# Kernel tuning notes

Hardware: AMD Instinct MI355X
Metric: run time of the kernel (lower is better)

## Reference

```python
import jax, jax.numpy as jnp
import numpy as np

B, T, D, H = 2, 1024, 1024, 16
K = D            # key_dim = hidden * expand_k (1.0)
V = 2 * D        # value_dim = hidden * expand_v (2.0)
DK, DV = K // H, V // H
I = 2816         # SwiGLU intermediate
CONV = 4
EPS = 1e-6


def rmsnorm(x, w, eps=EPS):
    return x * jax.lax.rsqrt(jnp.mean(x * x, -1, keepdims=True) + eps) * w


def l2norm(x, eps=EPS):
    return x * jax.lax.rsqrt(jnp.sum(x * x, -1, keepdims=True) + eps)


def short_conv(x, w):
    # depthwise causal conv1d (kernel CONV, no bias) + silu; x [B,T,C], w [C,CONV]
    kern = w.T[:, None, :]  # [CONV, 1, C]
    y = jax.lax.conv_general_dilated(
        x, kern, (1,), [(CONV - 1, 0)],
        dimension_numbers=('NWC', 'WIO', 'NWC'),
        feature_group_count=x.shape[-1])
    return jax.nn.silu(y)


def setup_inputs() -> dict:
    key = jax.random.key(0)
    ks = jax.random.split(key, 20)
    p = lambda i, shape, s=0.02: jax.random.normal(ks[i], shape, jnp.float32) * s
    return dict(
        x=jax.random.normal(ks[0], (B, T, D), jnp.float32),
        norm1_w=jnp.ones((D,), jnp.float32),
        wq=p(1, (D, K)), wk=p(2, (D, K)), wv=p(3, (D, V)),
        conv_q=p(4, (K, CONV), 0.3), conv_k=p(5, (K, CONV), 0.3), conv_v=p(6, (V, CONV), 0.3),
        wb=p(7, (D, H)), wa=p(8, (D, H)),
        A_log=jnp.log(jax.random.uniform(ks[9], (H,), jnp.float32, 1.0, 16.0)),
        dt_bias=jnp.log(jnp.expm1(jax.random.uniform(ks[10], (H,), jnp.float32, 0.001, 0.1))),
        wg=p(11, (D, V)),
        o_norm_w=jnp.ones((DV,), jnp.float32),
        wo=p(12, (V, D)),
        norm2_w=jnp.ones((D,), jnp.float32),
        w1=p(13, (D, I)), w2=p(14, (I, D)), w3=p(15, (D, I)),
    )


def reference(x, norm1_w, wq, wk, wv, conv_q, conv_k, conv_v, wb, wa,
              A_log, dt_bias, wg, o_norm_w, wo, norm2_w, w1, w2, w3):
    h = rmsnorm(x, norm1_w)
    # projections + short causal conv (silu)
    q = short_conv(h @ wq, conv_q).reshape(B, T, H, DK)
    k = short_conv(h @ wk, conv_k).reshape(B, T, H, DK)
    v = short_conv(h @ wv, conv_v).reshape(B, T, H, DV)
    q = l2norm(q) * (DK ** -0.5)
    k = l2norm(k)
    beta = jax.nn.sigmoid(h @ wb)                              # [B,T,H]
    # mamba-style decay gate: g = -exp(A_log) * softplus(a + dt_bias)
    g = -jnp.exp(A_log) * jax.nn.softplus(h @ wa + dt_bias)   # [B,T,H]

    # gated delta rule: S_t = exp(g_t)*S_{t-1}; u_t = beta_t*(v_t - k_t^T S_t);
    # S_t += k_t u_t^T; o_t = q_t^T S_t
    def step(S, inp):
        qt, kt, vt, gt, bt = inp                               # [B,H,*]
        S = S * jnp.exp(gt)[..., None, None]
        u = (vt - jnp.einsum('bhk,bhkv->bhv', kt, S)) * bt[..., None]
        S = S + kt[..., None] * u[:, :, None, :]
        ot = jnp.einsum('bhk,bhkv->bhv', qt, S)
        return S, ot

    S0 = jnp.zeros((B, H, DK, DV), x.dtype)
    seq = (q.transpose(1, 0, 2, 3), k.transpose(1, 0, 2, 3),
           v.transpose(1, 0, 2, 3), g.transpose(1, 0, 2), beta.transpose(1, 0, 2))
    _, o = jax.lax.scan(step, S0, seq)
    o = o.transpose(1, 0, 2, 3)                                # [B,T,H,DV]

    # output gate: per-head RMSNorm * swish(gate), then out-projection
    gate = (h @ wg).reshape(B, T, H, DV)
    o = rmsnorm(o, o_norm_w) * gate * jax.nn.sigmoid(gate)
    x = x + o.reshape(B, T, V) @ wo

    # SwiGLU MLP with residual
    h2 = rmsnorm(x, norm2_w)
    return x + (jax.nn.silu(h2 @ w1) * (h2 @ w3)) @ w2
```

## Files before the change

### kernel.cpp

```cpp
#include <hip/hip_runtime.h>
#include <stdint.h>

typedef unsigned short u16;
typedef float f32x4 __attribute__((ext_vector_type(4)));
typedef __bf16 bf16x8 __attribute__((ext_vector_type(8)));
typedef unsigned short u16x8 __attribute__((ext_vector_type(8)));

#define N1P 6400

__device__ __forceinline__ u16 f2bf(float f) {
    union { float f; uint32_t u; } v; v.f = f;
    uint32_t u = v.u;
    return (u16)((u + 0x7FFFu + ((u >> 16) & 1u)) >> 16);
}
__device__ __forceinline__ float bf2f(u16 h) {
    union { uint32_t u; float f; } v; v.u = ((uint32_t)h) << 16; return v.f;
}
__device__ __forceinline__ float sigm(float x) { return 1.f / (1.f + __expf(-x)); }

__device__ __forceinline__ void async16(const u16* g, u16* l) {
    __builtin_amdgcn_global_load_lds((const __attribute__((address_space(1))) void*)g,
                                     (__attribute__((address_space(3))) void*)l, 16, 0, 0);
}

__device__ __forceinline__ int swz64(int row, int col) {
    return row * 128 + ((((col >> 3) ^ (row & 7)) << 3) + (col & 7)) * 2;
}
__device__ __forceinline__ bf16x8 frag64(const u16* m, int rowbase, int lane, int kk) {
    const int row = rowbase + (lane & 15);
    const int unit = (lane >> 4) + (kk << 2);
    return *(const bf16x8*)((const char*)m + row * 128 + ((unit ^ (row & 7)) << 4));
}

struct TJob { const float* src; u16* dst; int rows, cols, rowOff, rowStride, nOut, blkBase, gx, mode; };
struct TJobs { TJob j[10]; };

__global__ __launch_bounds__(256) void k_transpose_all(TJobs jobs, int njobs) {
    __shared__ float tile[64][33];
    const int bid = blockIdx.x;
    int ji = 0;
#pragma unroll
    for (int i = 1; i < 10; ++i)
        if (i < njobs && bid >= jobs.j[i].blkBase) ji = i;
    const TJob J = jobs.j[ji];
    const int bx = bid - J.blkBase;
    const int n0 = (bx % J.gx) * 32, k0 = (bx / J.gx) * 64;
    const int tid = threadIdx.x;
    const int tx = tid & 31, ty = tid >> 5;
    const int c = n0 + tx;
    const bool cok = (c < J.cols);
#pragma unroll
    for (int i = 0; i < 8; ++i) {
        const int r = k0 + i * 8 + ty;
        tile[i * 8 + ty][tx] = cok ? J.src[(size_t)r * J.cols + c] : 0.f;
    }
    __syncthreads();
    const int n = tid >> 3, seg = tid & 7;
    const int ng = n0 + n;
    if (ng < J.nOut) {
        u16x8 o;
#pragma unroll
        for (int e = 0; e < 8; ++e) o[e] = f2bf(tile[seg * 8 + e][n]);
        const int drow = (J.mode == 0) ? (J.rowOff + ng * J.rowStride)
                                       : (J.rowOff + ((ng >> 4) << 5) + (ng & 15));
        *(u16x8*)&J.dst[(size_t)drow * J.rows + k0 + seg * 8] = o;
    }
}

__global__ __launch_bounds__(256) void k_rmsnorm(const float* __restrict__ x, const float* __restrict__ w,
                                                 u16* __restrict__ out) {
    const int row = blockIdx.x, tid = threadIdx.x, lane = tid & 63, wave = tid >> 6;
    const float4 v = ((const float4*)(x + (size_t)row * 1024))[tid];
    float ss = v.x * v.x + v.y * v.y + v.z * v.z + v.w * v.w;
#pragma unroll
    for (int o = 1; o < 64; o <<= 1) ss += __shfl_xor(ss, o);
    __shared__ float sred[4];
    if (lane == 0) sred[wave] = ss;
    __syncthreads();
    const float tot = sred[0] + sred[1] + sred[2] + sred[3];
    const float rn = rsqrtf(tot * (1.f / 1024.f) + 1e-6f);
    const float4 wv = ((const float4*)w)[tid];
    uint2 pk;
    pk.x = (uint32_t)f2bf(v.x * rn * wv.x) | ((uint32_t)f2bf(v.y * rn * wv.y) << 16);
    pk.y = (uint32_t)f2bf(v.z * rn * wv.z) | ((uint32_t)f2bf(v.w * rn * wv.w) << 16);
    *(uint2*)&out[(size_t)row * 1024 + tid * 4] = pk;
}

template <int EPI>
__global__ __launch_bounds__(512, 2) void k_gemm256(const u16* __restrict__ A, const u16* __restrict__ Bt,
                                                    u16* __restrict__ Cout, int N, int Kd) {
    __shared__ __align__(16) u16 L[65536];
    const int q8 = (int)gridDim.x >> 3;
    const int bid = blockIdx.x;
    const int wg = (bid & 7) * q8 + (bid >> 3);
    const int bm = wg & 7, bn = wg >> 3;
    const int tid = threadIdx.x, lane = tid & 63, wave = tid >> 6;
    const int wm = wave >> 2, wn = wave & 3;

    const int scol = ((tid & 7) ^ ((tid >> 3) & 7)) * 8;
    const u16* gA = A + (size_t)(bm * 256 + (tid >> 3)) * Kd + scol;
    const u16* gB = Bt + (size_t)(bn * 256 + (tid >> 3)) * Kd + scol;
    u16* dstT = L + tid * 8;

    const int NT = Kd >> 6;
    const int NI = NT >> 1;

    auto issue = [&](const u16* g, int mtx, int kt, int h) {
        u16* d = dstT + (kt & 1) * 32768 + mtx * 16384 + h * 8192;
        const u16* s = g + (size_t)(h * 128) * Kd + kt * 64;
        async16(s, d);
        async16(s + (size_t)64 * Kd, d + 4096);
    };

    issue(gB, 1, 0, 0); issue(gB, 1, 0, 1);
    issue(gA, 0, 0, 0); issue(gA, 0, 0, 1);
    issue(gB, 1, 1, 0); issue(gB, 1, 1, 1);
    asm volatile("s_waitcnt vmcnt(4)" ::: "memory");
    __builtin_amdgcn_s_barrier();

    f32x4 acc[8][4] = {};
    bf16x8 bq[4][2];

    for (int i = 0; i < NI; ++i) {
        const int kt0 = 2 * i;
#pragma unroll
        for (int p = 0; p < 8; ++p) {
            const int half = p >> 2;
            const int q = p & 3;
            const u16* Ab = L + half * 32768;
            const u16* Bb = L + half * 32768 + 16384;
            if (q == 0) {
#pragma unroll
                for (int ni = 0; ni < 4; ++ni)
#pragma unroll
                    for (int kk = 0; kk < 2; ++kk)
                        bq[ni][kk] = frag64(Bb, wn * 64 + ni * 16, lane, kk);
            }
            bf16x8 af[2][2];
#pragma unroll
            for (int j = 0; j < 2; ++j)
#pragma unroll
                for (int kk = 0; kk < 2; ++kk)
                    af[j][kk] = frag64(Ab, wm * 128 + (2 * q + j) * 16, lane, kk);
            if (p == 0) { if (kt0 + 1 < NT) issue(gA, 0, kt0 + 1, 0); }
            if (p == 1) { if (kt0 + 1 < NT) issue(gA, 0, kt0 + 1, 1);
                          if (kt0 + 2 < NT) issue(gB, 1, kt0 + 2, 0); }
            if (p == 2) { if (kt0 + 2 < NT) issue(gB, 1, kt0 + 2, 1); }
            if (p == 4) { if (kt0 + 2 < NT) issue(gA, 0, kt0 + 2, 0); }
            if (p == 5) { if (kt0 + 2 < NT) issue(gA, 0, kt0 + 2, 1);
                          if (kt0 + 3 < NT) issue(gB, 1, kt0 + 3, 0); }
            if (p == 6) { if (kt0 + 3 < NT) issue(gB, 1, kt0 + 3, 1); }
            if (p == 3) { if (i + 1 < NI) { asm volatile("s_waitcnt vmcnt(4)" ::: "memory"); }
                          else            { asm volatile("s_waitcnt vmcnt(0)" ::: "memory"); } }
            if (p == 7) { if (i + 1 < NI) { asm volatile("s_waitcnt vmcnt(4)" ::: "memory"); } }
            __builtin_amdgcn_s_barrier();
            __builtin_amdgcn_s_setprio(1);
#pragma unroll
            for (int j = 0; j < 2; ++j)
#pragma unroll
                for (int ni = 0; ni < 4; ++ni)
#pragma unroll
                    for (int kk = 0; kk < 2; ++kk)
                        acc[2 * q + j][ni] = __builtin_amdgcn_mfma_f32_16x16x32_bf16(
                            af[j][kk], bq[ni][kk], acc[2 * q + j][ni], 0, 0, 0);
            __builtin_amdgcn_s_setprio(0);
            __builtin_amdgcn_s_barrier();
        }
    }

    const int rsub = (lane >> 4) * 4, csub = lane & 15;
    if constexpr (EPI == 2) {
        u16* ct = L;
#pragma unroll
        for (int r = 0; r < 2; ++r) {
            if (wm == r) {
#pragma unroll
                for (int mi = 0; mi < 8; ++mi)
#pragma unroll
                    for (int ni = 0; ni < 4; ++ni)
#pragma unroll
                        for (int rr = 0; rr < 4; ++rr)
                            ct[(mi * 16 + rsub + rr) * 264 + wn * 64 + ni * 16 + csub] =
                                f2bf(acc[mi][ni][rr]);
            }
            __syncthreads();
#pragma unroll
            for (int k = 0; k < 8; ++k) {
                const int f = (tid + k * 512) * 8;
                const int r2 = f >> 8, c = f & 255;
                *(u16x8*)&Cout[(size_t)(bm * 256 + r * 128 + r2) * N + bn * 256 + c] =
                    *(const u16x8*)&ct[r2 * 264 + c];
            }
            __syncthreads();
        }
    } else {
        u16* ct = L;
#pragma unroll
        for (int mi = 0; mi < 8; ++mi)
#pragma unroll
            for (int g = 0; g < 2; ++g)
#pragma unroll
                for (int rr = 0; rr < 4; ++rr) {
                    const float u1 = acc[mi][2 * g][rr];
                    const float u3 = acc[mi][2 * g + 1][rr];
                    ct[(wm * 128 + mi * 16 + rsub + rr) * 132 + wn * 32 + g * 16 + csub] =
                        f2bf(u1 * sigm(u1) * u3);
                }
        __syncthreads();
#pragma unroll
        for (int k = 0; k < 8; ++k) {
            const int f = (tid + k * 512) * 8;
            const int r2 = f >> 7, c = f & 127;
            *(u16x8*)&Cout[(size_t)(bm * 256 + r2) * N + bn * 128 + c] =
                *(const u16x8*)&ct[r2 * 132 + c];
        }
    }
}

__global__ __launch_bounds__(512) void k_gemm_skinny(const u16* __restrict__ A, const u16* __restrict__ Bt,
                                                     float* __restrict__ Cout, const float* __restrict__ Res,
                                                     int N, int Kd) {
    __shared__ __align__(16) char smem[49152];
    u16* Asb = (u16*)smem;
    u16* Bsb = (u16*)(smem + 32768);
    const int q = (int)gridDim.x >> 3;
    const int bid = blockIdx.x;
    const int wg = (bid & 7) * q + (bid >> 3);
    const int bm = wg & 15, bn = wg >> 4;
    const int tid = threadIdx.x, lane = tid & 63, wave = tid >> 6;
    const int wm = wave >> 1, wn = wave & 1;

    const int srow = tid >> 3;
    const int scol = ((tid & 7) ^ ((tid >> 3) & 7)) * 8;
    const u16* gA = A + (size_t)(bm * 128 + srow) * Kd + scol;
    const u16* gB = Bt + (size_t)(bn * 64 + srow) * Kd + scol;

    f32x4 acc[2][2] = {};
    const int NT = Kd >> 6;

    async16(gA, Asb + wave * 512);
    async16(gA + (size_t)64 * Kd, Asb + 4096 + wave * 512);
    async16(gB, Bsb + wave * 512);
    asm volatile("s_waitcnt vmcnt(0)" ::: "memory");
    __syncthreads();

    int buf = 0;
    for (int t = 0; t < NT; ++t) {
        if (t + 1 < NT) {
            const int k0 = (t + 1) << 6;
            const int ba = (buf ^ 1) * 8192, bb2 = (buf ^ 1) * 4096;
            async16(gA + k0, Asb + ba + wave * 512);
            async16(gA + (size_t)64 * Kd + k0, Asb + ba + 4096 + wave * 512);
            async16(gB + k0, Bsb + bb2 + wave * 512);
        }
        const u16* Ab = Asb + buf * 8192;
        const u16* Bb = Bsb + buf * 4096;
#pragma unroll
        for (int kk = 0; kk < 2; ++kk) {
            bf16x8 af[2], bfr[2];
#pragma unroll
            for (int mi = 0; mi < 2; ++mi) af[mi] = frag64(Ab, wm * 32 + mi * 16, lane, kk);
#pragma unroll
            for (int ni = 0; ni < 2; ++ni) bfr[ni] = frag64(Bb, wn * 32 + ni * 16, lane, kk);
#pragma unroll
            for (int mi = 0; mi < 2; ++mi)
#pragma unroll
                for (int ni = 0; ni < 2; ++ni)
                    acc[mi][ni] = __builtin_amdgcn_mfma_f32_16x16x32_bf16(af[mi], bfr[ni], acc[mi][ni], 0, 0, 0);
        }
        asm volatile("s_waitcnt vmcnt(0)" ::: "memory");
        __syncthreads();
        buf ^= 1;
    }

    const int rsub = (lane >> 4) * 4;
    const int csub = lane & 15;
    float* ctile = (float*)smem;
#pragma unroll
    for (int mi = 0; mi < 2; ++mi)
#pragma unroll
        for (int ni = 0; ni < 2; ++ni)
#pragma unroll
            for (int r = 0; r < 4; ++r)
                ctile[(wm * 32 + mi * 16 + rsub + r) * 68 + wn * 32 + ni * 16 + csub] = acc[mi][ni][r];
    __syncthreads();
#pragma unroll
    for (int k = 0; k < 4; ++k) {
        const int f = (tid + k * 512) * 4;
        const int r = f >> 6, c = f & 63;
        float4 v = *(const float4*)&ctile[r * 68 + c];
        const float4 rv = *(const float4*)&Res[(size_t)(bm * 128 + r) * N + bn * 64 + c];
        v.x += rv.x; v.y += rv.y; v.z += rv.z; v.w += rv.w;
        *(float4*)&Cout[(size_t)(bm * 128 + r) * N + bn * 64 + c] = v;
    }
}

__global__ __launch_bounds__(256) void k_scan1(
    const u16* __restrict__ P, const float* __restrict__ cwq, const float* __restrict__ cwk,
    const float* __restrict__ cwv, const float* __restrict__ A_log, const float* __restrict__ dtb,
    u16* __restrict__ CHW, u16* __restrict__ CHM, u16* __restrict__ CHQc,
    u16* __restrict__ CHKcT, u16* __restrict__ CHU0T, float* __restrict__ CHcC,
    u16* __restrict__ CHA2m, u16* __restrict__ CHB) {
    __shared__ __align__(16) char sm[66048];
    u16* Ql   = (u16*)(sm);
    u16* Kl   = (u16*)(sm + 8192);
    u16* VTb  = (u16*)(sm + 16384);
    u16* KT1b = (u16*)(sm + 32768);
    u16* Mim  = (u16*)(sm + 40960);
    u16* MTim = (u16*)(sm + 49152);
    u16* Tb   = (u16*)(sm + 57344);
    float* Tl    = (float*)sm;
    float* gcs   = (float*)(sm + 65536);
    float* betal = (float*)(sm + 65792);
    u16* Vtmp = Mim;

    const int blk = blockIdx.x;
    const int bb = blk >> 8, h = (blk >> 4) & 15, ch = blk & 15;
    const int bhc = blk;
    const int tid = threadIdx.x, lane = tid & 63, wave = tid >> 6;
    const long rowbase = (long)bb * 1024 + ch * 64;

    if (tid < 64) {
        const long pr = (rowbase + tid) * (long)N1P;
        betal[tid] = sigm(bf2f(P[pr + 4096 + h]));
        const float a = bf2f(P[pr + 4112 + h]) + dtb[h];
        const float sp = (a > 15.f) ? a : log1pf(__expf(a));
        gcs[tid] = -__expf(A_log[h]) * sp;
    }
    {
        const int g = tid & 31, rb2 = tid >> 5;
        int colbase; const float* cw;
        if (g < 8)       { const int cc = h * 64 + g * 8;        colbase = cc;        cw = cwq + cc * 4; }
        else if (g < 16) { const int cc = h * 64 + (g - 8) * 8;   colbase = 1024 + cc; cw = cwk + cc * 4; }
        else             { const int cc = h * 128 + (g - 16) * 8; colbase = 2048 + cc; cw = cwv + cc * 4; }
        float4 wgt[8];
#pragma unroll
        for (int e = 0; e < 8; ++e) wgt[e] = ((const float4*)cw)[e];
        u16x8 taps[11];
#pragma unroll
        for (int j = 0; j < 11; ++j) {
            const int tloc = ch * 64 + rb2 * 8 - 3 + j;
            if (tloc >= 0) taps[j] = *(const u16x8*)&P[((long)bb * 1024 + tloc) * N1P + colbase];
            else           taps[j] = u16x8{};
        }
#pragma unroll
        for (int r = 0; r < 8; ++r) {
            float y[8];
            float ss = 0.f;
#pragma unroll
            for (int e = 0; e < 8; ++e) {
                float v = bf2f(taps[r][e]) * wgt[e].x + bf2f(taps[r + 1][e]) * wgt[e].y +
                          bf2f(taps[r + 2][e]) * wgt[e].z + bf2f(taps[r + 3][e]) * wgt[e].w;
                v = v * sigm(v);
                y[e] = v;
                ss += v * v;
            }
            ss += __shfl_xor(ss, 1); ss += __shfl_xor(ss, 2); ss += __shfl_xor(ss, 4);
            const float rn = rsqrtf(ss + 1e-6f);
            const float sc = (g < 8) ? rn * 0.125f : (g < 16 ? rn : 1.f);
            u16x8 o;
#pragma unroll
            for (int e = 0; e < 8; ++e) o[e] = f2bf(y[e] * sc);
            const int row = rb2 * 8 + r;
            if (g < 16) {
                u16* dst = (g < 8) ? Ql : Kl;
                *(u16x8*)((char*)dst + row * 128 + (((g & 7) ^ (row & 7)) << 4)) = o;
            } else {
                *(u16x8*)&Vtmp[row * 128 + (g - 16) * 8] = o;
            }
        }
    }
    __syncthreads();

    if (wave == 0) {
        float g = gcs[lane];
#pragma unroll
        for (int off = 1; off < 64; off <<= 1) {
            float n = __shfl_up(g, off, 64);
            if (lane >= off) g += n;
        }
        gcs[lane] = g;
    }
    for (int u = tid; u < 1024; u += 256) {
        int r = u >> 4, c8 = u & 15;
        u16x8 vv = *(const u16x8*)&Vtmp[r * 128 + c8 * 8];
        float bsc = betal[r];
#pragma unroll
        for (int j = 0; j < 8; ++j) {
            int dv = c8 * 8 + j;
            *(u16*)((char*)VTb + swz64(dv, r)) = f2bf(bf2f(vv[j]) * bsc);
        }
    }
    f32x4 aQK[4] = {}, aKK[4] = {};
#pragma unroll
    for (int nt = 0; nt < 4; ++nt)
#pragma unroll
        for (int kk = 0; kk < 2; ++kk) {
            bf16x8 bq = frag64(Kl, nt * 16, lane, kk);
            aQK[nt] = __builtin_amdgcn_mfma_f32_16x16x32_bf16(frag64(Ql, wave * 16, lane, kk), bq, aQK[nt], 0, 0, 0);
            aKK[nt] = __builtin_amdgcn_mfma_f32_16x16x32_bf16(frag64(Kl, wave * 16, lane, kk), bq, aKK[nt], 0, 0, 0);
        }
    __syncthreads();

    const float gcsC = gcs[63];
    float am[4][4];
#pragma unroll
    for (int nt = 0; nt < 4; ++nt)
#pragma unroll
        for (int reg = 0; reg < 4; ++reg) {
            int t = wave * 16 + ((lane >> 4) << 2) + reg;
            int i = nt * 16 + (lane & 15);
            float dec = __expf(gcs[t] - gcs[i]);
            float mv = (i <= t) ? dec * aQK[nt][reg] : 0.f;
            *(u16*)((char*)CHM + (size_t)bhc * 8192 + swz64(t, i)) = f2bf(mv);
            float a = (i < t) ? betal[t] * dec * aKK[nt][reg] : 0.f;
            am[nt][reg] = -a;
            u16 amb = f2bf(-a);
            *(u16*)((char*)Mim + swz64(t, i)) = amb;
            *(u16*)((char*)MTim + swz64(i, t)) = amb;
        }
    for (int e = tid; e < 4096; e += 256) {
        int r = e >> 6, c = e & 63;
        int ib = swz64(r, c);
        float qv = bf2f(*(const u16*)((const char*)Ql + ib)) * __expf(gcs[r]);
        *(u16*)((char*)CHQc + (size_t)bhc * 8192 + ib) = f2bf(qv);
        float kv = bf2f(*(const u16*)((const char*)Kl + ib));
        int ob = swz64(c, r);
        *(u16*)((char*)KT1b + ob) = f2bf(kv * betal[r] * __expf(gcs[r]));
        *(u16*)((char*)CHKcT + (size_t)bhc * 8192 + ob) = f2bf(kv * __expf(gcsC - gcs[r]));
    }
    if (tid == 0) CHcC[bhc] = __expf(gcsC);
    __syncthreads();

#pragma unroll
    for (int nt = 0; nt < 4; ++nt)
#pragma unroll
        for (int reg = 0; reg < 4; ++reg) {
            int t = wave * 16 + ((lane >> 4) << 2) + reg;
            int i = nt * 16 + (lane & 15);
            float tv = (t == i) ? 1.f : am[nt][reg];
            Tl[t * 64 + i] = tv;
            *(u16*)((char*)Tb + swz64(t, i)) = f2bf(tv);
        }
    __syncthreads();

    const int hi = wave * 16 + 15;
#pragma unroll
    for (int j = 1; j <= 5; ++j) {
        f32x4 aM[4] = {};
#pragma unroll
        for (int nt = 0; nt < 4; ++nt) {
            if (nt * 16 > hi - (1 << j)) continue;
#pragma unroll
            for (int kk = 0; kk < 2; ++kk) {
                if (kk * 32 > hi) break;
                aM[nt] = __builtin_amdgcn_mfma_f32_16x16x32_bf16(
                    frag64(Mim, wave * 16, lane, kk), frag64(MTim, nt * 16, lane, kk), aM[nt], 0, 0, 0);
            }
        }
        __syncthreads();
#pragma unroll
        for (int nt = 0; nt < 4; ++nt)
#pragma unroll
            for (int reg = 0; reg < 4; ++reg) {
                int t = wave * 16 + ((lane >> 4) << 2) + reg;
                int i = nt * 16 + (lane & 15);
                float mv = (t - i >= (1 << j)) ? aM[nt][reg] : 0.f;
                u16 mb = f2bf(mv);
                *(u16*)((char*)Mim + swz64(t, i)) = mb;
                *(u16*)((char*)MTim + swz64(i, t)) = mb;
            }
        __syncthreads();
        f32x4 aT[4];
#pragma unroll
        for (int nt = 0; nt < 4; ++nt)
#pragma unroll
            for (int reg = 0; reg < 4; ++reg) {
                int t = wave * 16 + ((lane >> 4) << 2) + reg;
                int i = nt * 16 + (lane & 15);
                aT[nt][reg] = Tl[t * 64 + i];
            }
#pragma unroll
        for (int nt = 0; nt < 4; ++nt) {
            if (nt * 16 > hi - (1 << j)) continue;
#pragma unroll
            for (int kk = 0; kk < 2; ++kk) {
                if (kk * 32 > hi) break;
                aT[nt] = __builtin_amdgcn_mfma_f32_16x16x32_bf16(
                    frag64(Tb, wave * 16, lane, kk), frag64(MTim, nt * 16, lane, kk), aT[nt], 0, 0, 0);
            }
        }
#pragma unroll
        for (int nt = 0; nt < 4; ++nt)
#pragma unroll
            for (int reg = 0; reg < 4; ++reg) {
                int t = wave * 16 + ((lane >> 4) << 2) + reg;
                int i = nt * 16 + (lane & 15);
                Tl[t * 64 + i] = aT[nt][reg];
                *(u16*)((char*)Tb + swz64(t, i)) = f2bf(aT[nt][reg]);
            }
    }
    __syncthreads();

    u16* KcTl = Ql;
    u16* WTl  = Kl;
    u16* U0Tl = Mim;
#pragma unroll
    for (int r = 0; r < 2; ++r) {
        const int g = r * 256 + tid;
        async16(CHKcT + (size_t)bhc * 4096 + (size_t)g * 8, KcTl + g * 8);
    }

    {
        f32x4 aW[4] = {};
#pragma unroll
        for (int nt = 0; nt < 4; ++nt)
#pragma unroll
            for (int kk = 0; kk < 2; ++kk) {
                if (kk * 32 > hi) break;
                aW[nt] = __builtin_amdgcn_mfma_f32_16x16x32_bf16(
                    frag64(Tb, wave * 16, lane, kk), frag64(KT1b, nt * 16, lane, kk), aW[nt], 0, 0, 0);
            }
#pragma unroll
        for (int nt = 0; nt < 4; ++nt)
#pragma unroll
            for (int reg = 0; reg < 4; ++reg) {
                int r = wave * 16 + ((lane >> 4) << 2) + reg;
                int c = nt * 16 + (lane & 15);
                u16 wv = f2bf(aW[nt][reg]);
                *(u16*)((char*)CHW + (size_t)bhc * 8192 + swz64(r, c)) = wv;
                *(u16*)((char*)WTl + swz64(c, r)) = wv;
            }
    }
#pragma unroll
    for (int rt = 0; rt < 2; ++rt) {
        f32x4 aU[4] = {};
        int rb = (wave * 2 + rt) * 16;
#pragma unroll
        for (int nt = 0; nt < 4; ++nt)
#pragma unroll
            for (int kk = 0; kk < 2; ++kk) {
                if (kk * 32 > nt * 16 + 15) continue;
                aU[nt] = __builtin_amdgcn_mfma_f32_16x16x32_bf16(
                    frag64(VTb, rb, lane, kk), frag64(Tb, nt * 16, lane, kk), aU[nt], 0, 0, 0);
            }
#pragma unroll
        for (int nt = 0; nt < 4; ++nt)
#pragma unroll
            for (int reg = 0; reg < 4; ++reg) {
                int dv = rb + ((lane >> 4) << 2) + reg;
                int c = nt * 16 + (lane & 15);
                u16 uv = f2bf(aU[nt][reg]);
                *(u16*)((char*)CHU0T + (size_t)bhc * 16384 + swz64(dv, c)) = uv;
                *(u16*)((char*)U0Tl + swz64(dv, c)) = uv;
            }
    }
    asm volatile("s_waitcnt vmcnt(0)" ::: "memory");
    __syncthreads();

    {
        f32x4 aA[4] = {};
#pragma unroll
        for (int nt = 0; nt < 4; ++nt)
#pragma unroll
            for (int kk = 0; kk < 2; ++kk)
                aA[nt] = __builtin_amdgcn_mfma_f32_16x16x32_bf16(
                    frag64(WTl, wave * 16, lane, kk), frag64(KcTl, nt * 16, lane, kk), aA[nt], 0, 0, 0);
#pragma unroll
        for (int nt = 0; nt < 4; ++nt)
#pragma unroll
            for (int reg = 0; reg < 4; ++reg) {
                int kI = wave * 16 + ((lane >> 4) << 2) + reg;
                int dk = nt * 16 + (lane & 15);
                *(u16*)((char*)CHA2m + (size_t)bhc * 8192 + swz64(dk, kI)) = f2bf(-aA[nt][reg]);
            }
    }
#pragma unroll
    for (int rt = 0; rt < 2; ++rt) {
        f32x4 aB[4] = {};
        int rb = (wave * 2 + rt) * 16;
#pragma unroll
        for (int nt = 0; nt < 4; ++nt)
#pragma unroll
            for (int kk = 0; kk < 2; ++kk)
                aB[nt] = __builtin_amdgcn_mfma_f32_16x16x32_bf16(
                    frag64(U0Tl, rb, lane, kk), frag64(KcTl, nt * 16, lane, kk), aB[nt], 0, 0, 0);
#pragma unroll
        for (int nt = 0; nt < 4; ++nt)
#pragma unroll
            for (int reg = 0; reg < 4; ++reg) {
                int dv = rb + ((lane >> 4) << 2) + reg;
                int dk = nt * 16 + (lane & 15);
                *(u16*)((char*)CHB + (size_t)bhc * 16384 + swz64(dv, dk)) = f2bf(aB[nt][reg]);
            }
    }
}

__global__ __launch_bounds__(256) void k_scan2(
    const u16* __restrict__ CHA2m, const u16* __restrict__ CHB,
    const float* __restrict__ CHcC, u16* __restrict__ CHS0) {
    __shared__ __align__(16) u16 stg[2][8192];
    __shared__ __align__(16) u16 STb[4096];
    __shared__ float ST[64 * 66];
    const int blk = blockIdx.x;
    const int bb = blk >> 5, h = (blk >> 1) & 15, dvh = blk & 1;
    const int bh = bb * 16 + h;
    const int tid = threadIdx.x, lane = tid & 63, wave = tid >> 6;

    for (int e = tid; e < 64 * 66; e += 256) ST[e] = 0.f;
    for (int e = tid; e < 4096; e += 256) STb[e] = 0;

    auto stage = [&](int buf, int ch) {
        const size_t base = (size_t)(bh * 16 + ch);
        const u16* sA = CHA2m + base * 4096;
        const u16* sB = CHB + base * 8192 + dvh * 4096;
#pragma unroll
        for (int r = 0; r < 2; ++r) {
            const int g = r * 256 + tid;
            async16(sA + (size_t)g * 8, &stg[buf][g * 8]);
            async16(sB + (size_t)g * 8, &stg[buf][4096 + g * 8]);
        }
    };
    stage(0, 0);
    int cur = 0;
    for (int ch = 0; ch < 16; ++ch) {
        asm volatile("s_waitcnt vmcnt(0)" ::: "memory");
        __syncthreads();
        if (ch < 15) stage(cur ^ 1, ch + 1);
        const u16* sA2 = &stg[cur][0];
        const u16* sB = &stg[cur][4096];
        f32x4 acc[4] = {};
#pragma unroll
        for (int nt = 0; nt < 4; ++nt)
#pragma unroll
            for (int kk = 0; kk < 2; ++kk)
                acc[nt] = __builtin_amdgcn_mfma_f32_16x16x32_bf16(
                    frag64(STb, wave * 16, lane, kk), frag64(sA2, nt * 16, lane, kk), acc[nt], 0, 0, 0);
        const float cC = CHcC[bh * 16 + ch];
        const size_t sbase = ((size_t)(bh * 16 + ch + 1) * 2 + dvh) * 8192;
#pragma unroll
        for (int nt = 0; nt < 4; ++nt)
#pragma unroll
            for (int reg = 0; reg < 4; ++reg) {
                const int rr = wave * 16 + ((lane >> 4) << 2) + reg;
                const int cc = nt * 16 + (lane & 15);
                const float bv = bf2f(*(const u16*)((const char*)sB + swz64(rr, cc)));
                const float ns = cC * ST[rr * 66 + cc] + acc[nt][reg] + bv;
                ST[rr * 66 + cc] = ns;
                const u16 nb = f2bf(ns);
                *(u16*)((char*)STb + swz64(rr, cc)) = nb;
                if (ch < 15) *(u16*)((char*)CHS0 + sbase + swz64(rr, cc)) = nb;
            }
        cur ^= 1;
    }
}

__global__ __launch_bounds__(256) void k_scan3(
    const u16* __restrict__ CHM, const u16* __restrict__ CHQc, const u16* __restrict__ CHW,
    const u16* __restrict__ CHU0T, const u16* __restrict__ CHS0, const u16* __restrict__ P,
    const float* __restrict__ onw, u16* __restrict__ OG) {
    __shared__ __align__(16) char sm3[73728];
    u16* sM  = (u16*)sm3;
    u16* sQc = (u16*)(sm3 + 8192);
    u16* sW  = (u16*)(sm3 + 16384);
    u16* sU  = (u16*)(sm3 + 24576);
    u16* sS0 = (u16*)(sm3 + 40960);
    u16* sPg = (u16*)(sm3 + 57344);
    const int blk = blockIdx.x;
    const int bb = blk >> 8, h = (blk >> 4) & 15, ch = blk & 15;
    const size_t bhc = blk;
    const int tid = threadIdx.x, lane = tid & 63, wave = tid >> 6;
    const bool hasS0 = (ch != 0);

#pragma unroll
    for (int r = 0; r < 2; ++r) {
        const int g = r * 256 + tid;
        async16(CHM + bhc * 4096 + (size_t)g * 8, sM + g * 8);
        async16(CHQc + bhc * 4096 + (size_t)g * 8, sQc + g * 8);
        async16(CHW + bhc * 4096 + (size_t)g * 8, sW + g * 8);
#pragma unroll
        for (int d = 0; d < 2; ++d) {
            async16(CHU0T + (bhc * 2 + d) * 4096 + (size_t)g * 8, sU + d * 4096 + g * 8);
            if (hasS0)
                async16(CHS0 + (bhc * 2 + d) * 4096 + (size_t)g * 8, sS0 + d * 4096 + g * 8);
        }
    }
    const long prow0 = ((long)bb * 1024 + ch * 64) * N1P + 4128 + h * 128;
#pragma unroll
    for (int k = 0; k < 4; ++k) {
        const int i = tid + k * 256;
        const int row = i >> 4, seg = i & 15;
        async16(P + prow0 + (long)row * N1P + seg * 8, sPg + i * 8);
    }
    asm volatile("s_waitcnt vmcnt(0)" ::: "memory");
    __syncthreads();

    if (hasS0) {
#pragma unroll
        for (int d = 0; d < 2; ++d) {
            f32x4 au[4] = {};
#pragma unroll
            for (int nt = 0; nt < 4; ++nt)
#pragma unroll
                for (int kk = 0; kk < 2; ++kk)
                    au[nt] = __builtin_amdgcn_mfma_f32_16x16x32_bf16(
                        frag64(sS0 + d * 4096, wave * 16, lane, kk), frag64(sW, nt * 16, lane, kk),
                        au[nt], 0, 0, 0);
#pragma unroll
            for (int nt = 0; nt < 4; ++nt)
#pragma unroll
                for (int reg = 0; reg < 4; ++reg) {
                    const int dv = wave * 16 + ((lane >> 4) << 2) + reg;
                    const int c = nt * 16 + (lane & 15);
                    u16* p = (u16*)((char*)sU + d * 8192 + swz64(dv, c));
                    *p = f2bf(bf2f(*p) - au[nt][reg]);
                }
        }
        __syncthreads();
    }

    f32x4 accO[2][4] = {};
#pragma unroll
    for (int d = 0; d < 2; ++d)
#pragma unroll
        for (int nt = 0; nt < 4; ++nt)
#pragma unroll
            for (int kk = 0; kk < 2; ++kk) {
                accO[d][nt] = __builtin_amdgcn_mfma_f32_16x16x32_bf16(
                    frag64(sM, wave * 16, lane, kk), frag64(sU + d * 4096, nt * 16, lane, kk),
                    accO[d][nt], 0, 0, 0);
                if (hasS0)
                    accO[d][nt] = __builtin_amdgcn_mfma_f32_16x16x32_bf16(
                        frag64(sQc, wave * 16, lane, kk), frag64(sS0 + d * 4096, nt * 16, lane, kk),
                        accO[d][nt], 0, 0, 0);
            }

    const int rsub = (lane >> 4) * 4, csub = lane & 15;
    float rn[4];
#pragma unroll
    for (int reg = 0; reg < 4; ++reg) {
        float ss = 0.f;
#pragma unroll
        for (int d = 0; d < 2; ++d)
#pragma unroll
            for (int nt = 0; nt < 4; ++nt) {
                const float v = accO[d][nt][reg];
                ss += v * v;
            }
        ss += __shfl_xor(ss, 1); ss += __shfl_xor(ss, 2);
        ss += __shfl_xor(ss, 4); ss += __shfl_xor(ss, 8);
        rn[reg] = rsqrtf(ss * (1.f / 128.f) + 1e-6f);
    }
    __syncthreads();
    u16* ct = (u16*)sm3;
#pragma unroll
    for (int d = 0; d < 2; ++d)
#pragma unroll
        for (int nt = 0; nt < 4; ++nt)
#pragma unroll
            for (int reg = 0; reg < 4; ++reg) {
                const int rr = wave * 16 + rsub + reg;
                const int dv = d * 64 + nt * 16 + csub;
                const float g = bf2f(sPg[rr * 128 + dv]);
                const float val = accO[d][nt][reg] * rn[reg] * onw[dv] * g * sigm(g);
                ct[rr * 136 + dv] = f2bf(val);
            }
    __syncthreads();
#pragma unroll
    for (int k = 0; k < 4; ++k) {
        const int f = (tid + k * 256) * 8;
        const int r2 = f >> 7, c = f & 127;
        *(u16x8*)&OG[(size_t)(bb * 1024 + ch * 64 + r2) * 2048 + h * 128 + c] =
            *(const u16x8*)&ct[r2 * 136 + c];
    }
}

extern "C" void kernel_launch(void* const* d_in, const int* in_sizes, int n_in,
                              void* d_out, int out_size, void* d_ws, size_t ws_size,
                              hipStream_t stream) {
    const float* x   = (const float*)d_in[0];
    const float* n1w = (const float*)d_in[1];
    const float* wq  = (const float*)d_in[2];
    const float* wk  = (const float*)d_in[3];
    const float* wv  = (const float*)d_in[4];
    const float* cq  = (const float*)d_in[5];
    const float* ck  = (const float*)d_in[6];
    const float* cv  = (const float*)d_in[7];
    const float* wb  = (const float*)d_in[8];
    const float* wa  = (const float*)d_in[9];
    const float* Alg = (const float*)d_in[10];
    const float* dtb = (const float*)d_in[11];
    const float* wg  = (const float*)d_in[12];
    const float* onw = (const float*)d_in[13];
    const float* wo  = (const float*)d_in[14];
    const float* n2w = (const float*)d_in[15];
    const float* w1  = (const float*)d_in[16];
    const float* w2  = (const float*)d_in[17];
    const float* w3  = (const float*)d_in[18];

    if (ws_size < 132384768ULL) return;

    char* ws = (char*)d_ws;
    u16*   WcatT = (u16*)(ws + 0);
    u16*   WoT   = (u16*)(ws + 13107200);
    u16*   W13T  = (u16*)(ws + 17301504);
    u16*   W2T   = (u16*)(ws + 28835840);
    u16*   hA    = (u16*)(ws + 34603008);
    u16*   P     = (u16*)(ws + 38797312);
    u16*   Mm    = (u16*)(ws + 65011712);
    u16*   OG    = (u16*)(ws + 73400320);
    float* X2    = (float*)(ws + 82051072);
    u16*   CHKcT = (u16*)(ws + 98828288);
    u16*   CHU0T = (u16*)(ws + 103022592);
    float* CHcC  = (float*)(ws + 111411200);
    u16*   CHA2m = (u16*)(ws + 111413248);
    u16*   CHB   = (u16*)(ws + 115607552);
    u16*   CHS0  = (u16*)(ws + 123996160);
    u16*   CHW   = WcatT;
    u16*   CHM   = (u16*)(ws + 4194304);
    u16*   CHQc  = (u16*)(ws + 8388608);
    u16*   h2A = hA;

    TJobs tj;
    tj.j[0] = { wq, WcatT, 1024, 1024,    0, 1, 1024,     0, 32, 0 };
    tj.j[1] = { wk, WcatT, 1024, 1024, 1024, 1, 1024,   512, 32, 0 };
    tj.j[2] = { wv, WcatT, 1024, 2048, 2048, 1, 2048,  1024, 64, 0 };
    tj.j[3] = { wb, WcatT, 1024,   16, 4096, 1,   16,  2048,  1, 0 };
    tj.j[4] = { wa, WcatT, 1024,   16, 4112, 1,   16,  2064,  1, 0 };
    tj.j[5] = { wg, WcatT, 1024, 2048, 4128, 1, 2272,  2080, 71, 0 };
    tj.j[6] = { wo, WoT,   2048, 1024,    0, 1, 1024,  3216, 32, 0 };
    tj.j[7] = { w1, W13T,  1024, 2816,    0, 1, 2816,  4240, 88, 1 };
    tj.j[8] = { w3, W13T,  1024, 2816,   16, 1, 2816,  5648, 88, 1 };
    tj.j[9] = { w2, W2T,   2816, 1024,    0, 1, 1024,  7056, 32, 0 };
    k_transpose_all<<<8464, 256, 0, stream>>>(tj, 10);

    k_rmsnorm<<<2048, 256, 0, stream>>>(x, n1w, hA);
    k_gemm256<2><<<200, 512, 0, stream>>>(hA, WcatT, P, N1P, 1024);

    k_scan1<<<512, 256, 0, stream>>>(P, cq, ck, cv, Alg, dtb, CHW, CHM, CHQc, CHKcT, CHU0T,
                                     CHcC, CHA2m, CHB);
    k_scan2<<<64, 256, 0, stream>>>(CHA2m, CHB, CHcC, CHS0);
    k_scan3<<<512, 256, 0, stream>>>(CHM, CHQc, CHW, CHU0T, CHS0, P, onw, OG);

    k_gemm_skinny<<<256, 512, 0, stream>>>(OG, WoT, X2, x, 1024, 2048);

    k_rmsnorm<<<2048, 256, 0, stream>>>(X2, n2w, h2A);
    k_gemm256<3><<<176, 512, 0, stream>>>(h2A, W13T, Mm, 2816, 1024);
    k_gemm_skinny<<<256, 512, 0, stream>>>(Mm, W2T, (float*)d_out, X2, 1024, 2816);
}
```

Measured before the change: 222.1 us.

## Fuse first RMSNorm into transpose launch and keep KcT chunk tile in LDS

```diff
diff --git a/kernel.cpp b/kernel.cpp
--- a/kernel.cpp
+++ b/kernel.cpp
@@ -5,6 +5,7 @@
 typedef float f32x4 __attribute__((ext_vector_type(4)));
 typedef __bf16 bf16x8 __attribute__((ext_vector_type(8)));
 typedef unsigned short u16x8 __attribute__((ext_vector_type(8)));
+typedef unsigned short u16x4 __attribute__((ext_vector_type(4)));
 
 #define N1P 6400
 
@@ -35,9 +36,32 @@
 struct TJob { const float* src; u16* dst; int rows, cols, rowOff, rowStride, nOut, blkBase, gx, mode; };
 struct TJobs { TJob j[10]; };
 
-__global__ __launch_bounds__(256) void k_transpose_all(TJobs jobs, int njobs) {
+__global__ __launch_bounds__(256) void k_transpose_all(TJobs jobs, int njobs, int rmsBase,
+                                                       const float* __restrict__ xin,
+                                                       const float* __restrict__ n1w,
+                                                       u16* __restrict__ hOut) {
     __shared__ float tile[64][33];
     const int bid = blockIdx.x;
+    const int tid = threadIdx.x;
+    if (bid >= rmsBase) {
+        const int row = bid - rmsBase;
+        const int lane = tid & 63, wave = tid >> 6;
+        const float4 v = ((const float4*)(xin + (size_t)row * 1024))[tid];
+        float ss = v.x * v.x + v.y * v.y + v.z * v.z + v.w * v.w;
+#pragma unroll
+        for (int o = 1; o < 64; o <<= 1) ss += __shfl_xor(ss, o);
+        float* sred = &tile[0][0];
+        if (lane == 0) sred[wave] = ss;
+        __syncthreads();
+        const float tot = sred[0] + sred[1] + sred[2] + sred[3];
+        const float rn = rsqrtf(tot * (1.f / 1024.f) + 1e-6f);
+        const float4 wv = ((const float4*)n1w)[tid];
+        uint2 pk;
+        pk.x = (uint32_t)f2bf(v.x * rn * wv.x) | ((uint32_t)f2bf(v.y * rn * wv.y) << 16);
+        pk.y = (uint32_t)f2bf(v.z * rn * wv.z) | ((uint32_t)f2bf(v.w * rn * wv.w) << 16);
+        *(uint2*)&hOut[(size_t)row * 1024 + tid * 4] = pk;
+        return;
+    }
     int ji = 0;
 #pragma unroll
     for (int i = 1; i < 10; ++i)
@@ -45,7 +69,6 @@
     const TJob J = jobs.j[ji];
     const int bx = bid - J.blkBase;
     const int n0 = (bx % J.gx) * 32, k0 = (bx / J.gx) * 64;
-    const int tid = threadIdx.x;
     const int tx = tid & 31, ty = tid >> 5;
     const int c = n0 + tx;
     const bool cok = (c < J.cols);
@@ -299,9 +322,9 @@
     const u16* __restrict__ P, const float* __restrict__ cwq, const float* __restrict__ cwk,
     const float* __restrict__ cwv, const float* __restrict__ A_log, const float* __restrict__ dtb,
     u16* __restrict__ CHW, u16* __restrict__ CHM, u16* __restrict__ CHQc,
-    u16* __restrict__ CHKcT, u16* __restrict__ CHU0T, float* __restrict__ CHcC,
+    u16* __restrict__ CHU0T, float* __restrict__ CHcC,
     u16* __restrict__ CHA2m, u16* __restrict__ CHB) {
-    __shared__ __align__(16) char sm[66048];
+    __shared__ __align__(16) char sm[75008];
     u16* Ql   = (u16*)(sm);
     u16* Kl   = (u16*)(sm + 8192);
     u16* VTb  = (u16*)(sm + 16384);
@@ -309,9 +332,13 @@
     u16* Mim  = (u16*)(sm + 40960);
     u16* MTim = (u16*)(sm + 49152);
     u16* Tb   = (u16*)(sm + 57344);
+    u16* KcTl = (u16*)(sm + 65536);
     float* Tl    = (float*)sm;
-    float* gcs   = (float*)(sm + 65536);
-    float* betal = (float*)(sm + 65792);
+    float* gcs   = (float*)(sm + 73728);
+    float* betal = (float*)(sm + 73984);
+    float* egcs  = (float*)(sm + 74240);
+    float* egcsC = (float*)(sm + 74496);
+    float* bkc   = (float*)(sm + 74752);
     u16* Vtmp = Mim;
 
     const int blk = blockIdx.x;
@@ -319,6 +346,7 @@
     const int bhc = blk;
     const int tid = threadIdx.x, lane = tid & 63, wave = tid >> 6;
     const long rowbase = (long)bb * 1024 + ch * 64;
+    const int tbase = wave * 16 + ((lane >> 4) << 2);
 
     if (tid < 64) {
         const long pr = (rowbase + tid) * (long)N1P;
@@ -380,6 +408,11 @@
             if (lane >= off) g += n;
         }
         gcs[lane] = g;
+        const float gC = __shfl(g, 63);
+        const float eg = __expf(g);
+        egcs[lane] = eg;
+        egcsC[lane] = __expf(gC - g);
+        bkc[lane] = betal[lane] * eg;
     }
     for (int u = tid; u < 1024; u += 256) {
         int r = u >> 4, c8 = u & 15;
@@ -402,43 +435,45 @@
         }
     __syncthreads();
 
-    const float gcsC = gcs[63];
     float am[4][4];
 #pragma unroll
+    for (int nt = 0; nt < 4; ++nt) {
+        const int i = nt * 16 + (lane & 15);
+        u16x4 mtv;
+#pragma unroll
+        for (int reg = 0; reg < 4; ++reg) {
+            const int t = tbase + reg;
+            const float dec = __expf(gcs[t] - gcs[i]);
+            const float mv = (i <= t) ? dec * aQK[nt][reg] : 0.f;
+            *(u16*)((char*)CHM + (size_t)bhc * 8192 + swz64(t, i)) = f2bf(mv);
+            const float a = (i < t) ? betal[t] * dec * aKK[nt][reg] : 0.f;
+            am[nt][reg] = -a;
+            const u16 amb = f2bf(-a);
+            *(u16*)((char*)Mim + swz64(t, i)) = amb;
+            mtv[reg] = amb;
+        }
+        *(u16x4*)((char*)MTim + i * 128 + ((((tbase >> 3) ^ (i & 7)) << 4) + (tbase & 7) * 2)) = mtv;
+    }
+    for (int e = tid; e < 4096; e += 256) {
+        const int r = e >> 6, c = e & 63;
+        const int ib = swz64(r, c);
+        const float qv = bf2f(*(const u16*)((const char*)Ql + ib)) * egcs[r];
+        *(u16*)((char*)CHQc + (size_t)bhc * 8192 + ib) = f2bf(qv);
+        const float kv = bf2f(*(const u16*)((const char*)Kl + ib));
+        const int ob = swz64(c, r);
+        *(u16*)((char*)KT1b + ob) = f2bf(kv * bkc[r]);
+        *(u16*)((char*)KcTl + ob) = f2bf(kv * egcsC[r]);
+    }
+    if (tid == 0) CHcC[bhc] = egcs[63];
+    __syncthreads();
+
+#pragma unroll
     for (int nt = 0; nt < 4; ++nt)
 #pragma unroll
         for (int reg = 0; reg < 4; ++reg) {
-            int t = wave * 16 + ((lane >> 4) << 2) + reg;
-            int i = nt * 16 + (lane & 15);
-            float dec = __expf(gcs[t] - gcs[i]);
-            float mv = (i <= t) ? dec * aQK[nt][reg] : 0.f;
-            *(u16*)((char*)CHM + (size_t)bhc * 8192 + swz64(t, i)) = f2bf(mv);
-            float a = (i < t) ? betal[t] * dec * aKK[nt][reg] : 0.f;
-            am[nt][reg] = -a;
-            u16 amb = f2bf(-a);
-            *(u16*)((char*)Mim + swz64(t, i)) = amb;
-            *(u16*)((char*)MTim + swz64(i, t)) = amb;
-        }
-    for (int e = tid; e < 4096; e += 256) {
-        int r = e >> 6, c = e & 63;
-        int ib = swz64(r, c);
-        float qv = bf2f(*(const u16*)((const char*)Ql + ib)) * __expf(gcs[r]);
-        *(u16*)((char*)CHQc + (size_t)bhc * 8192 + ib) = f2bf(qv);
-        float kv = bf2f(*(const u16*)((const char*)Kl + ib));
-        int ob = swz64(c, r);
-        *(u16*)((char*)KT1b + ob) = f2bf(kv * betal[r] * __expf(gcs[r]));
-        *(u16*)((char*)CHKcT + (size_t)bhc * 8192 + ob) = f2bf(kv * __expf(gcsC - gcs[r]));
-    }
-    if (tid == 0) CHcC[bhc] = __expf(gcsC);
-    __syncthreads();
-
-#pragma unroll
-    for (int nt = 0; nt < 4; ++nt)
-#pragma unroll
-        for (int reg = 0; reg < 4; ++reg) {
-            int t = wave * 16 + ((lane >> 4) << 2) + reg;
-            int i = nt * 16 + (lane & 15);
-            float tv = (t == i) ? 1.f : am[nt][reg];
+            const int t = tbase + reg;
+            const int i = nt * 16 + (lane & 15);
+            const float tv = (t == i) ? 1.f : am[nt][reg];
             Tl[t * 64 + i] = tv;
             *(u16*)((char*)Tb + swz64(t, i)) = f2bf(tv);
         }
@@ -460,26 +495,26 @@
         }
         __syncthreads();
 #pragma unroll
-        for (int nt = 0; nt < 4; ++nt)
+        for (int nt = 0; nt < 4; ++nt) {
+            const int i = nt * 16 + (lane & 15);
+            u16x4 mtv;
 #pragma unroll
             for (int reg = 0; reg < 4; ++reg) {
-                int t = wave * 16 + ((lane >> 4) << 2) + reg;
-                int i = nt * 16 + (lane & 15);
-                float mv = (t - i >= (1 << j)) ? aM[nt][reg] : 0.f;
-                u16 mb = f2bf(mv);
+                const int t = tbase + reg;
+                const float mv = (t - i >= (1 << j)) ? aM[nt][reg] : 0.f;
+                const u16 mb = f2bf(mv);
                 *(u16*)((char*)Mim + swz64(t, i)) = mb;
-                *(u16*)((char*)MTim + swz64(i, t)) = mb;
-            }
+                mtv[reg] = mb;
+            }
+            *(u16x4*)((char*)MTim + i * 128 + ((((tbase >> 3) ^ (i & 7)) << 4) + (tbase & 7) * 2)) = mtv;
+        }
         __syncthreads();
         f32x4 aT[4];
 #pragma unroll
         for (int nt = 0; nt < 4; ++nt)
 #pragma unroll
-            for (int reg = 0; reg < 4; ++reg) {
-                int t = wave * 16 + ((lane >> 4) << 2) + reg;
-                int i = nt * 16 + (lane & 15);
-                aT[nt][reg] = Tl[t * 64 + i];
-            }
+            for (int reg = 0; reg < 4; ++reg)
+                aT[nt][reg] = Tl[(tbase + reg) * 64 + nt * 16 + (lane & 15)];
 #pragma unroll
         for (int nt = 0; nt < 4; ++nt) {
             if (nt * 16 > hi - (1 << j)) continue;
@@ -494,22 +529,16 @@
         for (int nt = 0; nt < 4; ++nt)
 #pragma unroll
             for (int reg = 0; reg < 4; ++reg) {
-                int t = wave * 16 + ((lane >> 4) << 2) + reg;
-                int i = nt * 16 + (lane & 15);
+                const int t = tbase + reg;
+                const int i = nt * 16 + (lane & 15);
                 Tl[t * 64 + i] = aT[nt][reg];
                 *(u16*)((char*)Tb + swz64(t, i)) = f2bf(aT[nt][reg]);
             }
     }
     __syncthreads();
 
-    u16* KcTl = Ql;
     u16* WTl  = Kl;
     u16* U0Tl = Mim;
-#pragma unroll
-    for (int r = 0; r < 2; ++r) {
-        const int g = r * 256 + tid;
-        async16(CHKcT + (size_t)bhc * 4096 + (size_t)g * 8, KcTl + g * 8);
-    }
 
     {
         f32x4 aW[4] = {};
@@ -522,20 +551,23 @@
                     frag64(Tb, wave * 16, lane, kk), frag64(KT1b, nt * 16, lane, kk), aW[nt], 0, 0, 0);
             }
 #pragma unroll
-        for (int nt = 0; nt < 4; ++nt)
+        for (int nt = 0; nt < 4; ++nt) {
+            const int c = nt * 16 + (lane & 15);
+            u16x4 wtv;
 #pragma unroll
             for (int reg = 0; reg < 4; ++reg) {
-                int r = wave * 16 + ((lane >> 4) << 2) + reg;
-                int c = nt * 16 + (lane & 15);
-                u16 wv = f2bf(aW[nt][reg]);
+                const int r = tbase + reg;
+                const u16 wv = f2bf(aW[nt][reg]);
                 *(u16*)((char*)CHW + (size_t)bhc * 8192 + swz64(r, c)) = wv;
-                *(u16*)((char*)WTl + swz64(c, r)) = wv;
-            }
+                wtv[reg] = wv;
+            }
+            *(u16x4*)((char*)WTl + c * 128 + ((((tbase >> 3) ^ (c & 7)) << 4) + (tbase & 7) * 2)) = wtv;
+        }
     }
 #pragma unroll
     for (int rt = 0; rt < 2; ++rt) {
         f32x4 aU[4] = {};
-        int rb = (wave * 2 + rt) * 16;
+        const int rb = (wave * 2 + rt) * 16;
 #pragma unroll
         for (int nt = 0; nt < 4; ++nt)
 #pragma unroll
@@ -548,14 +580,13 @@
         for (int nt = 0; nt < 4; ++nt)
 #pragma unroll
             for (int reg = 0; reg < 4; ++reg) {
-                int dv = rb + ((lane >> 4) << 2) + reg;
-                int c = nt * 16 + (lane & 15);
-                u16 uv = f2bf(aU[nt][reg]);
+                const int dv = rb + ((lane >> 4) << 2) + reg;
+                const int c = nt * 16 + (lane & 15);
+                const u16 uv = f2bf(aU[nt][reg]);
                 *(u16*)((char*)CHU0T + (size_t)bhc * 16384 + swz64(dv, c)) = uv;
                 *(u16*)((char*)U0Tl + swz64(dv, c)) = uv;
             }
     }
-    asm volatile("s_waitcnt vmcnt(0)" ::: "memory");
     __syncthreads();
 
     {
@@ -567,18 +598,19 @@
                 aA[nt] = __builtin_amdgcn_mfma_f32_16x16x32_bf16(
                     frag64(WTl, wave * 16, lane, kk), frag64(KcTl, nt * 16, lane, kk), aA[nt], 0, 0, 0);
 #pragma unroll
-        for (int nt = 0; nt < 4; ++nt)
-#pragma unroll
-            for (int reg = 0; reg < 4; ++reg) {
-                int kI = wave * 16 + ((lane >> 4) << 2) + reg;
-                int dk = nt * 16 + (lane & 15);
-                *(u16*)((char*)CHA2m + (size_t)bhc * 8192 + swz64(dk, kI)) = f2bf(-aA[nt][reg]);
-            }
+        for (int nt = 0; nt < 4; ++nt) {
+            const int dk = nt * 16 + (lane & 15);
+            u16x4 av;
+#pragma unroll
+            for (int reg = 0; reg < 4; ++reg) av[reg] = f2bf(-aA[nt][reg]);
+            *(u16x4*)((char*)CHA2m + (size_t)bhc * 8192 + dk * 128 +
+                      ((((tbase >> 3) ^ (dk & 7)) << 4) + (tbase & 7) * 2)) = av;
+        }
     }
 #pragma unroll
     for (int rt = 0; rt < 2; ++rt) {
         f32x4 aB[4] = {};
-        int rb = (wave * 2 + rt) * 16;
+        const int rb = (wave * 2 + rt) * 16;
 #pragma unroll
         for (int nt = 0; nt < 4; ++nt)
 #pragma unroll
@@ -589,8 +621,8 @@
         for (int nt = 0; nt < 4; ++nt)
 #pragma unroll
             for (int reg = 0; reg < 4; ++reg) {
-                int dv = rb + ((lane >> 4) << 2) + reg;
-                int dk = nt * 16 + (lane & 15);
+                const int dv = rb + ((lane >> 4) << 2) + reg;
+                const int dk = nt * 16 + (lane & 15);
                 *(u16*)((char*)CHB + (size_t)bhc * 16384 + swz64(dv, dk)) = f2bf(aB[nt][reg]);
             }
     }
@@ -810,7 +842,6 @@
     u16*   Mm    = (u16*)(ws + 65011712);
     u16*   OG    = (u16*)(ws + 73400320);
     float* X2    = (float*)(ws + 82051072);
-    u16*   CHKcT = (u16*)(ws + 98828288);
     u16*   CHU0T = (u16*)(ws + 103022592);
     float* CHcC  = (float*)(ws + 111411200);
     u16*   CHA2m = (u16*)(ws + 111413248);
@@ -832,12 +863,11 @@
     tj.j[7] = { w1, W13T,  1024, 2816,    0, 1, 2816,  4240, 88, 1 };
     tj.j[8] = { w3, W13T,  1024, 2816,   16, 1, 2816,  5648, 88, 1 };
     tj.j[9] = { w2, W2T,   2816, 1024,    0, 1, 1024,  7056, 32, 0 };
-    k_transpose_all<<<8464, 256, 0, stream>>>(tj, 10);
-
-    k_rmsnorm<<<2048, 256, 0, stream>>>(x, n1w, hA);
+    k_transpose_all<<<8464 + 2048, 256, 0, stream>>>(tj, 10, 8464, x, n1w, hA);
+
     k_gemm256<2><<<200, 512, 0, stream>>>(hA, WcatT, P, N1P, 1024);
 
-    k_scan1<<<512, 256, 0, stream>>>(P, cq, ck, cv, Alg, dtb, CHW, CHM, CHQc, CHKcT, CHU0T,
+    k_scan1<<<512, 256, 0, stream>>>(P, cq, ck, cv, Alg, dtb, CHW, CHM, CHQc, CHU0T,
                                      CHcC, CHA2m, CHB);
     k_scan2<<<64, 256, 0, stream>>>(CHA2m, CHB, CHcC, CHS0);
     k_scan3<<<512, 256, 0, stream>>>(CHM, CHQc, CHW, CHU0T, CHS0, P, onw, OG);
```

Measured after the change: 217.5 us. 1.02x faster.
